# Kernel optimization log

Measured on AMD Instinct MI355X. Metric: run time of the kernel, lower is better.

## Reference

```python
import jax, jax.numpy as jnp
import numpy as np


def setup_inputs() -> dict:
    key = jax.random.key(0)
    k1, k2, k3, k4 = jax.random.split(key, 4)
    B, N, F_in, F_out = 8, 2048, 256, 256
    inp = jax.random.normal(k1, (B, N, F_in), dtype=jnp.float32)
    adj = jax.random.uniform(k2, (B, N, N), dtype=jnp.float32)
    stdv = 1.0 / np.sqrt(F_out)
    weight = jax.random.uniform(k3, (F_in, F_out), dtype=jnp.float32, minval=-stdv, maxval=stdv)
    bias = jax.random.uniform(k4, (F_out,), dtype=jnp.float32, minval=-stdv, maxval=stdv)
    return {"input": inp, "adj": adj, "weight": weight, "bias": bias}


def reference(input, adj, weight, bias):
    # d = (sum over dim 1 of adj) ** -0.5, matching torch adj.sum(dim=1)
    d = adj.sum(axis=1) ** -0.5  # [B, N]
    # D @ A @ D with diagonal D -> row/col broadcast scaling (same math)
    adj_norm = d[:, :, None] * adj * d[:, None, :]  # [B, N, N]
    support = jnp.einsum('bnf,fo->bno', input, weight)  # [B, N, F_out]
    output = jnp.einsum('bnm,bmo->bno', adj_norm, support) + bias
    return output
```

## Files before the change

kernel.cpp:

```cpp
#include <hip/hip_runtime.h>
#include <hip/hip_bf16.h>

#define BATCH 8
#define NDIM 2048
#define FDIM 256
#define CH 32

typedef float f32x4 __attribute__((ext_vector_type(4)));
typedef short bf16x8 __attribute__((ext_vector_type(8)));
typedef short bf16x4 __attribute__((ext_vector_type(4)));

__device__ __forceinline__ short f2bf(float f) {
  __hip_bfloat16 h = __float2bfloat16(f);
  short s;
  __builtin_memcpy(&s, &h, 2);
  return s;
}

__device__ __forceinline__ void gload_lds16(const void* g, void* l) {
  __builtin_amdgcn_global_load_lds(
      (const __attribute__((address_space(1))) void*)g,
      (__attribute__((address_space(3))) void*)l, 16, 0, 0);
}

__global__ __launch_bounds__(256) void k_colsum(const float* __restrict__ adj,
                                                float* __restrict__ part) {
  int bid = blockIdx.x;
  int cb = bid & 1;
  int ch = (bid >> 1) & (CH - 1);
  int b = bid >> 6;
  int col = cb * 1024 + threadIdx.x * 4;
  const float* p = adj + (size_t)b * NDIM * NDIM + (size_t)(ch * 64) * NDIM + col;
  f32x4 acc = {0.f, 0.f, 0.f, 0.f};
#pragma unroll 8
  for (int i = 0; i < 64; ++i) acc += *(const f32x4*)(p + (size_t)i * NDIM);
  *(f32x4*)(part + (size_t)(b * CH + ch) * NDIM + col) = acc;
}

__global__ __launch_bounds__(256) void k_small(const float* __restrict__ part,
                                               float* __restrict__ dnorm,
                                               const float* __restrict__ w,
                                               short* __restrict__ wt) {
  int t = threadIdx.x;
  if (blockIdx.x < 64) {
    int idx = blockIdx.x * 256 + t;
    int b = idx >> 11, j = idx & (NDIM - 1);
    float s = 0.f;
#pragma unroll
    for (int c = 0; c < CH; ++c) s += part[(size_t)(b * CH + c) * NDIM + j];
    dnorm[idx] = rsqrtf(s);
  } else {
    __shared__ float tile[64][65];
    int bb = blockIdx.x - 64;
    int bx = bb & 3, by = bb >> 2;
    int f0 = by * 64, o0 = bx * 64;
    int c4 = 4 * (t & 15);
#pragma unroll
    for (int q = 0; q < 4; ++q) {
      int r = (t >> 4) + 16 * q;
      f32x4 v = *(const f32x4*)(w + (size_t)(f0 + r) * FDIM + o0 + c4);
#pragma unroll
      for (int i = 0; i < 4; ++i) tile[r][c4 + i] = v[i];
    }
    __syncthreads();
#pragma unroll
    for (int q = 0; q < 4; ++q) {
      int r = (t >> 4) + 16 * q;
      bf16x4 pk;
#pragma unroll
      for (int i = 0; i < 4; ++i) pk[i] = f2bf(tile[c4 + i][r]);
      *(bf16x4*)(wt + (size_t)(o0 + r) * FDIM + f0 + c4) = pk;
    }
  }
}

__global__ __launch_bounds__(256) void k_support(const float* __restrict__ in,
                                                 const short* __restrict__ wt,
                                                 const float* __restrict__ dnorm,
                                                 short* __restrict__ st) {
  __shared__ short Al[64 * 32];
  __shared__ short Bl[256 * 32];
  int t = threadIdx.x, lane = t & 63, w = t >> 6;
  int b = blockIdx.x >> 5;
  int m0 = (blockIdx.x & 31) * 64;
  const float* inb = in + ((size_t)b * NDIM + m0) * FDIM;

  f32x4 acc[4][4];
#pragma unroll
  for (int m = 0; m < 4; ++m)
#pragma unroll
    for (int n = 0; n < 4; ++n) acc[m][n] = {0.f, 0.f, 0.f, 0.f};

  int ar = t >> 2, ac = t & 3;
  for (int it = 0; it < 8; ++it) {
    int k0 = it * 32;
    {
      f32x4 v0 = *(const f32x4*)(inb + (size_t)ar * FDIM + k0 + 8 * ac);
      f32x4 v1 = *(const f32x4*)(inb + (size_t)ar * FDIM + k0 + 8 * ac + 4);
      bf16x8 p;
#pragma unroll
      for (int i = 0; i < 4; ++i) { p[i] = f2bf(v0[i]); p[4 + i] = f2bf(v1[i]); }
      *(bf16x8*)&Al[ar * 32 + 8 * ac] = p;
    }
#pragma unroll
    for (int i = 0; i < 4; ++i) {
      int ss = i * 256 + t;
      int o = ss >> 2, c = ss & 3;
      gload_lds16(wt + (size_t)o * FDIM + k0 + 8 * c, &Bl[ss * 8]);
    }
    __syncthreads();
    bf16x8 af[4], bf[4];
#pragma unroll
    for (int m = 0; m < 4; ++m)
      af[m] = *(const bf16x8*)&Al[(16 * m + (lane & 15)) * 32 + (lane >> 4) * 8];
#pragma unroll
    for (int n = 0; n < 4; ++n)
      bf[n] = *(const bf16x8*)&Bl[(64 * w + 16 * n + (lane & 15)) * 32 + (lane >> 4) * 8];
#pragma unroll
    for (int m = 0; m < 4; ++m)
#pragma unroll
      for (int n = 0; n < 4; ++n)
        acc[m][n] = __builtin_amdgcn_mfma_f32_16x16x32_bf16(af[m], bf[n], acc[m][n], 0, 0, 0);
    __syncthreads();
  }
#pragma unroll
  for (int m = 0; m < 4; ++m) {
    int row = m0 + 16 * m + ((lane >> 4) << 2);
    float dm[4];
#pragma unroll
    for (int j = 0; j < 4; ++j) dm[j] = dnorm[b * NDIM + row + j];
#pragma unroll
    for (int n = 0; n < 4; ++n) {
      int col = 64 * w + 16 * n + (lane & 15);
      bf16x4 pk;
#pragma unroll
      for (int j = 0; j < 4; ++j) pk[j] = f2bf(acc[m][n][j] * dm[j]);
      *(bf16x4*)(st + ((size_t)(b * FDIM + col)) * NDIM + row) = pk;
    }
  }
}

__global__ __launch_bounds__(512) void k_main(const float* __restrict__ adj,
                                              const short* __restrict__ st,
                                              const float* __restrict__ dnorm,
                                              const float* __restrict__ bias,
                                              float* __restrict__ out) {
  __shared__ float Alf[3][64 * 64];
  __shared__ short Bl[3][256 * 64];
  int t = threadIdx.x, lane = t & 63, w = t >> 6;
  int wm = w & 1, wn = w >> 1;
  int b = blockIdx.x & 7;
  int n0 = (blockIdx.x >> 3) * 64;
  const float* ab = adj + ((size_t)b * NDIM + n0) * NDIM;
  const short* stb = st + (size_t)b * FDIM * NDIM;

  int s0 = t, s1 = 512 + t;
  int r0 = s0 >> 4, c0 = (s0 & 15) ^ ((r0 & 7) << 1);
  int r1 = s1 >> 4, c1 = (s1 & 15) ^ ((r1 & 7) << 1);
  const float* a0s = ab + (size_t)r0 * NDIM + c0 * 4;
  const float* a1s = ab + (size_t)r1 * NDIM + c1 * 4;
  int arow = t >> 3;
  int schk = (t & 7) ^ (arow & 7);
  const short* bsrc = stb + (size_t)arow * NDIM + 8 * schk;

  f32x4 acc[2][4];
#pragma unroll
  for (int m = 0; m < 2; ++m)
#pragma unroll
    for (int n = 0; n < 4; ++n) acc[m][n] = {0.f, 0.f, 0.f, 0.f};

  int lr = lane & 15, kg = lane >> 4, sw = lane & 7, sw2 = (lane & 7) << 1;

  auto stage = [&](int k, int bp) {
    int kc = k > 31 ? 31 : k;
    size_t ko = (size_t)kc * 64;
    gload_lds16(a0s + ko, &Alf[bp][s0 * 4]);
    gload_lds16(a1s + ko, &Alf[bp][s1 * 4]);
#pragma unroll
    for (int i = 0; i < 4; ++i)
      gload_lds16(bsrc + (size_t)(i * 64) * NDIM + ko, &Bl[bp][(i * 512 + t) * 8]);
  };

  auto body = [&](int it, int bc, int bp) {
    stage(it + 2, bp);
    asm volatile("s_waitcnt vmcnt(12)" ::: "memory");
    __builtin_amdgcn_s_barrier();
    asm volatile("" ::: "memory");
    __builtin_amdgcn_sched_barrier(0);
#pragma unroll
    for (int h = 0; h < 2; ++h) {
      int gk = h * 4 + kg;
      bf16x8 af[2];
#pragma unroll
      for (int mf = 0; mf < 2; ++mf) {
        const float* ap = &Alf[bc][(wm * 32 + mf * 16 + lr) * 64 + (((2 * gk) ^ sw2) * 4)];
        f32x4 lo = *(const f32x4*)ap;
        f32x4 hi = *(const f32x4*)(ap + 4);
#pragma unroll
        for (int j = 0; j < 4; ++j) { af[mf][j] = f2bf(lo[j]); af[mf][4 + j] = f2bf(hi[j]); }
      }
      int kc = (gk ^ sw) * 8;
      bf16x8 bv0 = *(const bf16x8*)&Bl[bc][(wn * 64 + lr) * 64 + kc];
      bf16x8 bv1 = *(const bf16x8*)&Bl[bc][(wn * 64 + 16 + lr) * 64 + kc];
      bf16x8 bv2 = *(const bf16x8*)&Bl[bc][(wn * 64 + 32 + lr) * 64 + kc];
      bf16x8 bv3 = *(const bf16x8*)&Bl[bc][(wn * 64 + 48 + lr) * 64 + kc];
      acc[0][0] = __builtin_amdgcn_mfma_f32_16x16x32_bf16(af[0], bv0, acc[0][0], 0, 0, 0);
      acc[0][1] = __builtin_amdgcn_mfma_f32_16x16x32_bf16(af[0], bv1, acc[0][1], 0, 0, 0);
      acc[0][2] = __builtin_amdgcn_mfma_f32_16x16x32_bf16(af[0], bv2, acc[0][2], 0, 0, 0);
      acc[0][3] = __builtin_amdgcn_mfma_f32_16x16x32_bf16(af[0], bv3, acc[0][3], 0, 0, 0);
      acc[1][0] = __builtin_amdgcn_mfma_f32_16x16x32_bf16(af[1], bv0, acc[1][0], 0, 0, 0);
      acc[1][1] = __builtin_amdgcn_mfma_f32_16x16x32_bf16(af[1], bv1, acc[1][1], 0, 0, 0);
      acc[1][2] = __builtin_amdgcn_mfma_f32_16x16x32_bf16(af[1], bv2, acc[1][2], 0, 0, 0);
      acc[1][3] = __builtin_amdgcn_mfma_f32_16x16x32_bf16(af[1], bv3, acc[1][3], 0, 0, 0);
    }
    asm volatile("s_waitcnt lgkmcnt(0)" ::: "memory");
    __builtin_amdgcn_s_barrier();
    asm volatile("" ::: "memory");
  };

  stage(0, 0);
  stage(1, 1);

  for (int itb = 0; itb < 30; itb += 3) {
    body(itb + 0, 0, 2);
    body(itb + 1, 1, 0);
    body(itb + 2, 2, 1);
  }
  body(30, 0, 2);
  body(31, 1, 0);

#pragma unroll
  for (int mf = 0; mf < 2; ++mf) {
    int row = n0 + wm * 32 + mf * 16 + kg * 4;
    f32x4 dr = *(const f32x4*)&dnorm[b * NDIM + row];
#pragma unroll
    for (int nf = 0; nf < 4; ++nf) {
      int col = wn * 64 + nf * 16 + lr;
      float bv = bias[col];
      float* op = out + ((size_t)b * NDIM + row) * FDIM + col;
#pragma unroll
      for (int j = 0; j < 4; ++j) op[(size_t)j * FDIM] = dr[j] * acc[mf][nf][j] + bv;
    }
  }
}

extern "C" void kernel_launch(void* const* d_in, const int* in_sizes, int n_in,
                              void* d_out, int out_size, void* d_ws, size_t ws_size,
                              hipStream_t stream) {
  (void)in_sizes; (void)n_in; (void)out_size; (void)ws_size;
  const float* input = (const float*)d_in[0];
  const float* adj = (const float*)d_in[1];
  const float* weight = (const float*)d_in[2];
  const float* bias = (const float*)d_in[3];
  float* out = (float*)d_out;

  char* ws = (char*)d_ws;
  short* st = (short*)ws;
  float* dnorm = (float*)(ws + 8ull * 1024 * 1024);
  float* part = (float*)(ws + 8ull * 1024 * 1024 + 65536);
  short* wt = (short*)(ws + 8ull * 1024 * 1024 + 65536 + 2ull * 1024 * 1024);

  k_colsum<<<dim3(BATCH * CH * 2), dim3(256), 0, stream>>>(adj, part);
  k_small<<<dim3(80), dim3(256), 0, stream>>>(part, dnorm, weight, wt);
  k_support<<<dim3(BATCH * (NDIM / 64)), dim3(256), 0, stream>>>(input, wt, dnorm, st);
  k_main<<<dim3(BATCH * (NDIM / 64)), dim3(512), 0, stream>>>(adj, st, dnorm, bias, out);
}
```

Baseline: 76.46 us.

## Split k_main output columns across two blocks with double buffering

The main aggregation kernel now splits the 256 output features into two halves, launching twice as many blocks, each computing a 64x128 tile. LDS staging drops from triple to double buffering and the B tile halves, cutting shared memory per block so more blocks can be resident (launch_bounds min 4). The cost is that each adj row tile is now read twice from global memory and converted to bf16 twice, with less prefetch depth to hide load latency.

```diff
diff --git a/kernel.cpp b/kernel.cpp
--- a/kernel.cpp
+++ b/kernel.cpp
@@ -140,78 +140,80 @@
   }
 }
 
-__global__ __launch_bounds__(512) void k_main(const float* __restrict__ adj,
-                                              const short* __restrict__ st,
-                                              const float* __restrict__ dnorm,
-                                              const float* __restrict__ bias,
-                                              float* __restrict__ out) {
-  __shared__ float Alf[3][64 * 64];
-  __shared__ short Bl[3][256 * 64];
+__global__ __launch_bounds__(512, 4) void k_main(const float* __restrict__ adj,
+                                                 const short* __restrict__ st,
+                                                 const float* __restrict__ dnorm,
+                                                 const float* __restrict__ bias,
+                                                 float* __restrict__ out) {
+  __shared__ float Alf[2][64 * 64];
+  __shared__ short Bl[2][128 * 64];
   int t = threadIdx.x, lane = t & 63, w = t >> 6;
   int wm = w & 1, wn = w >> 1;
   int b = blockIdx.x & 7;
-  int n0 = (blockIdx.x >> 3) * 64;
+  int rc = blockIdx.x >> 3;
+  int colh = rc & 1;
+  int n0 = (rc >> 1) * 64;
   const float* ab = adj + ((size_t)b * NDIM + n0) * NDIM;
-  const short* stb = st + (size_t)b * FDIM * NDIM;
-
-  int s0 = t, s1 = 512 + t;
-  int r0 = s0 >> 4, c0 = (s0 & 15) ^ ((r0 & 7) << 1);
-  int r1 = s1 >> 4, c1 = (s1 & 15) ^ ((r1 & 7) << 1);
-  const float* a0s = ab + (size_t)r0 * NDIM + c0 * 4;
-  const float* a1s = ab + (size_t)r1 * NDIM + c1 * 4;
-  int arow = t >> 3;
-  int schk = (t & 7) ^ (arow & 7);
-  const short* bsrc = stb + (size_t)arow * NDIM + 8 * schk;
-
-  f32x4 acc[2][4];
+  const short* stb = st + (size_t)b * FDIM * NDIM + (size_t)(colh * 128) * NDIM;
+
+  int sA0 = t, sA1 = 512 + t;
+  int rA0 = sA0 >> 4, cA0 = sA0 & 15;
+  int rA1 = sA1 >> 4, cA1 = sA1 & 15;
+  int cA0s = (((cA0 >> 1) ^ (rA0 & 7)) << 1) | (cA0 & 1);
+  int cA1s = (((cA1 >> 1) ^ (rA1 & 7)) << 1) | (cA1 & 1);
+  const float* aS0 = ab + (size_t)rA0 * NDIM + cA0s * 4;
+  const float* aS1 = ab + (size_t)rA1 * NDIM + cA1s * 4;
+  int sB0 = t, sB1 = 512 + t;
+  int rB0 = sB0 >> 3, cB0 = (sB0 & 7) ^ (rB0 & 7);
+  int rB1 = sB1 >> 3, cB1 = (sB1 & 7) ^ (rB1 & 7);
+  const short* bS0 = stb + (size_t)rB0 * NDIM + cB0 * 8;
+  const short* bS1 = stb + (size_t)rB1 * NDIM + cB1 * 8;
+
+  f32x4 acc[2][2];
 #pragma unroll
   for (int m = 0; m < 2; ++m)
 #pragma unroll
-    for (int n = 0; n < 4; ++n) acc[m][n] = {0.f, 0.f, 0.f, 0.f};
-
-  int lr = lane & 15, kg = lane >> 4, sw = lane & 7, sw2 = (lane & 7) << 1;
+    for (int n = 0; n < 2; ++n) acc[m][n] = {0.f, 0.f, 0.f, 0.f};
+
+  int lr = lane & 15, kg = lane >> 4, sw = lane & 7;
 
   auto stage = [&](int k, int bp) {
-    int kc = k > 31 ? 31 : k;
-    size_t ko = (size_t)kc * 64;
-    gload_lds16(a0s + ko, &Alf[bp][s0 * 4]);
-    gload_lds16(a1s + ko, &Alf[bp][s1 * 4]);
-#pragma unroll
-    for (int i = 0; i < 4; ++i)
-      gload_lds16(bsrc + (size_t)(i * 64) * NDIM + ko, &Bl[bp][(i * 512 + t) * 8]);
+    size_t ko = (size_t)k * 64;
+    gload_lds16(aS0 + ko, &Alf[bp][sA0 * 4]);
+    gload_lds16(aS1 + ko, &Alf[bp][sA1 * 4]);
+    gload_lds16(bS0 + ko, &Bl[bp][sB0 * 8]);
+    gload_lds16(bS1 + ko, &Bl[bp][sB1 * 8]);
   };
 
-  auto body = [&](int it, int bc, int bp) {
-    stage(it + 2, bp);
-    asm volatile("s_waitcnt vmcnt(12)" ::: "memory");
+  auto body = [&](int it, int bc, bool last) {
+    if (!last) {
+      stage(it + 1, bc ^ 1);
+      asm volatile("s_waitcnt vmcnt(4)" ::: "memory");
+    } else {
+      asm volatile("s_waitcnt vmcnt(0)" ::: "memory");
+    }
     __builtin_amdgcn_s_barrier();
     asm volatile("" ::: "memory");
     __builtin_amdgcn_sched_barrier(0);
 #pragma unroll
     for (int h = 0; h < 2; ++h) {
       int gk = h * 4 + kg;
+      int gsw = (gk ^ sw) * 8;
       bf16x8 af[2];
 #pragma unroll
       for (int mf = 0; mf < 2; ++mf) {
-        const float* ap = &Alf[bc][(wm * 32 + mf * 16 + lr) * 64 + (((2 * gk) ^ sw2) * 4)];
+        const float* ap = &Alf[bc][(wm * 32 + mf * 16 + lr) * 64 + gsw];
         f32x4 lo = *(const f32x4*)ap;
         f32x4 hi = *(const f32x4*)(ap + 4);
 #pragma unroll
         for (int j = 0; j < 4; ++j) { af[mf][j] = f2bf(lo[j]); af[mf][4 + j] = f2bf(hi[j]); }
       }
-      int kc = (gk ^ sw) * 8;
-      bf16x8 bv0 = *(const bf16x8*)&Bl[bc][(wn * 64 + lr) * 64 + kc];
-      bf16x8 bv1 = *(const bf16x8*)&Bl[bc][(wn * 64 + 16 + lr) * 64 + kc];
-      bf16x8 bv2 = *(const bf16x8*)&Bl[bc][(wn * 64 + 32 + lr) * 64 + kc];
-      bf16x8 bv3 = *(const bf16x8*)&Bl[bc][(wn * 64 + 48 + lr) * 64 + kc];
+      bf16x8 bv0 = *(const bf16x8*)&Bl[bc][(wn * 32 + lr) * 64 + gsw];
+      bf16x8 bv1 = *(const bf16x8*)&Bl[bc][(wn * 32 + 16 + lr) * 64 + gsw];
       acc[0][0] = __builtin_amdgcn_mfma_f32_16x16x32_bf16(af[0], bv0, acc[0][0], 0, 0, 0);
       acc[0][1] = __builtin_amdgcn_mfma_f32_16x16x32_bf16(af[0], bv1, acc[0][1], 0, 0, 0);
-      acc[0][2] = __builtin_amdgcn_mfma_f32_16x16x32_bf16(af[0], bv2, acc[0][2], 0, 0, 0);
-      acc[0][3] = __builtin_amdgcn_mfma_f32_16x16x32_bf16(af[0], bv3, acc[0][3], 0, 0, 0);
       acc[1][0] = __builtin_amdgcn_mfma_f32_16x16x32_bf16(af[1], bv0, acc[1][0], 0, 0, 0);
       acc[1][1] = __builtin_amdgcn_mfma_f32_16x16x32_bf16(af[1], bv1, acc[1][1], 0, 0, 0);
-      acc[1][2] = __builtin_amdgcn_mfma_f32_16x16x32_bf16(af[1], bv2, acc[1][2], 0, 0, 0);
-      acc[1][3] = __builtin_amdgcn_mfma_f32_16x16x32_bf16(af[1], bv3, acc[1][3], 0, 0, 0);
     }
     asm volatile("s_waitcnt lgkmcnt(0)" ::: "memory");
     __builtin_amdgcn_s_barrier();
@@ -219,23 +221,16 @@
   };
 
   stage(0, 0);
-  stage(1, 1);
-
-  for (int itb = 0; itb < 30; itb += 3) {
-    body(itb + 0, 0, 2);
-    body(itb + 1, 1, 0);
-    body(itb + 2, 2, 1);
-  }
-  body(30, 0, 2);
-  body(31, 1, 0);
+  for (int it = 0; it < 31; ++it) body(it, it & 1, false);
+  body(31, 1, true);
 
 #pragma unroll
   for (int mf = 0; mf < 2; ++mf) {
     int row = n0 + wm * 32 + mf * 16 + kg * 4;
     f32x4 dr = *(const f32x4*)&dnorm[b * NDIM + row];
 #pragma unroll
-    for (int nf = 0; nf < 4; ++nf) {
-      int col = wn * 64 + nf * 16 + lr;
+    for (int nf = 0; nf < 2; ++nf) {
+      int col = colh * 128 + wn * 32 + nf * 16 + lr;
       float bv = bias[col];
       float* op = out + ((size_t)b * NDIM + row) * FDIM + col;
 #pragma unroll
@@ -263,5 +258,5 @@
   k_colsum<<<dim3(BATCH * CH * 2), dim3(256), 0, stream>>>(adj, part);
   k_small<<<dim3(80), dim3(256), 0, stream>>>(part, dnorm, weight, wt);
   k_support<<<dim3(BATCH * (NDIM / 64)), dim3(256), 0, stream>>>(input, wt, dnorm, st);
-  k_main<<<dim3(BATCH * (NDIM / 64)), dim3(512), 0, stream>>>(adj, st, dnorm, bias, out);
-}
+  k_main<<<dim3(BATCH * (NDIM / 32)), dim3(512), 0, stream>>>(adj, st, dnorm, bias, out);
+}
```

Result: no change. 76.66 us (+0.3%).
